# Kernel optimization log

Hardware: AMD Instinct MI355X
Metric: run time of the kernel (lower is better)

## Reference

```python
import jax, jax.numpy as jnp
import numpy as np

B, S, D = 2, 2048, 1024
H, DH = 16, 64  # H*DH == D


def setup_inputs() -> dict:
    key = jax.random.key(0)
    ks = jax.random.split(key, 7)
    scale = 1.0 / np.sqrt(D)
    return {
        "x": jax.random.normal(ks[0], (B, S, D), dtype=jnp.float32),
        "mask": jax.random.normal(ks[1], (B, 1, 1, S), dtype=jnp.float32),
        "Wq": jax.random.normal(ks[2], (D, D), dtype=jnp.float32) * scale,
        "Wk": jax.random.normal(ks[3], (D, D), dtype=jnp.float32) * scale,
        "Wv": jax.random.normal(ks[4], (D, D), dtype=jnp.float32) * scale,
        "Wo": jax.random.normal(ks[5], (D, D), dtype=jnp.float32) * scale,
        "bo": jax.random.normal(ks[6], (D,), dtype=jnp.float32) * 0.01,
    }


def reference(x, mask, Wq, Wk, Wv, Wo, bo):
    # QKV projections (bias-free), split heads: [B,S,D] -> [B,H,S,DH]
    def split_heads(t):
        return t.reshape(B, S, H, DH).transpose(0, 2, 1, 3)

    q = split_heads(x @ Wq)
    k = split_heads(x @ Wk)
    v = split_heads(x @ Wv)

    # NOTE: module scales by sqrt(input_dim), not sqrt(head_size)
    scores = jnp.einsum("bhqd,bhkd->bhqk", q, k) / jnp.sqrt(jnp.float32(D))
    scores = scores + mask  # additive mask, broadcast [B,1,1,S]
    attn = jax.nn.softmax(scores, axis=-1)
    ctx = jnp.einsum("bhqk,bhkd->bhqd", attn, v)  # [B,H,S,DH]
    ctx = ctx.transpose(0, 2, 1, 3).reshape(B, S, H * DH)
    return ctx @ Wo + bo
```

## Files before the change

kernel.cpp:

```cpp
#include <hip/hip_runtime.h>
#include <hip/hip_bf16.h>

#define BB 2
#define SS 2048
#define DD 1024
#define HH 16
#define DHD 64
#define QKLD 2048

typedef __attribute__((ext_vector_type(8))) __bf16 bf16x8;
typedef __attribute__((ext_vector_type(4))) __bf16 bf16x4;
typedef __attribute__((ext_vector_type(4))) float f32x4;

__device__ __forceinline__ f32x4 mfma16(bf16x8 a, bf16x8 b, f32x4 c) {
  return __builtin_amdgcn_mfma_f32_16x16x32_bf16(a, b, c, 0, 0, 0);
}
__device__ __forceinline__ void gload_lds16(const void* g, void* l) {
  __builtin_amdgcn_global_load_lds((__attribute__((address_space(1))) const void*)g,
                                   (__attribute__((address_space(3))) void*)l, 16, 0, 0);
}

__global__ __launch_bounds__(256) void cast_x_em_kernel(
    const float* __restrict__ in, __bf16* __restrict__ out,
    const float* __restrict__ mask, __bf16* __restrict__ embf, int n4) {
  int i = blockIdx.x * 256 + threadIdx.x;
  if (i < n4) {
    float4 f = ((const float4*)in)[i];
    bf16x4 o;
    o[0] = (__bf16)f.x; o[1] = (__bf16)f.y; o[2] = (__bf16)f.z; o[3] = (__bf16)f.w;
    *(bf16x4*)(out + (size_t)i * 4) = o;
  } else {
    int j = i - n4;
    if (j < BB * SS) embf[j] = (__bf16)__expf(mask[j]);
  }
}

__global__ __launch_bounds__(256) void wtrans4_kernel(
    const float* __restrict__ Wq, const float* __restrict__ Wk,
    const float* __restrict__ Wv, const float* __restrict__ Wo,
    __bf16* __restrict__ WTbase) {
  int z = blockIdx.z;
  const float* W = (z == 0) ? Wq : (z == 1) ? Wk : (z == 2) ? Wv : Wo;
  __bf16* WT = WTbase + ((size_t)z << 20);
  __shared__ __bf16 t[64][65];
  int c0 = blockIdx.x * 64, r0 = blockIdx.y * 64;
  int tid = threadIdx.x;
  {
    int rr = tid >> 4, cg = tid & 15;
#pragma unroll
    for (int it = 0; it < 4; ++it) {
      int r = rr + it * 16;
      float4 f = *(const float4*)(W + (size_t)(r0 + r) * DD + c0 + cg * 4);
      t[r][cg * 4 + 0] = (__bf16)f.x;
      t[r][cg * 4 + 1] = (__bf16)f.y;
      t[r][cg * 4 + 2] = (__bf16)f.z;
      t[r][cg * 4 + 3] = (__bf16)f.w;
    }
  }
  __syncthreads();
  {
    int sg = tid & 7;
#pragma unroll
    for (int it = 0; it < 2; ++it) {
      int wc = (tid >> 3) + it * 32;
      __bf16 tmp[8];
#pragma unroll
      for (int e = 0; e < 8; ++e) tmp[e] = t[sg * 8 + e][wc];
      bf16x8 o;
#pragma unroll
      for (int e = 0; e < 8; ++e) o[e] = tmp[e];
      *(bf16x8*)(WT + (size_t)(c0 + wc) * DD + r0 + sg * 8) = o;
    }
  }
}

template <int MODE>
__global__ __launch_bounds__(256, 2) void gemm128_kernel(
    const __bf16* __restrict__ A, const __bf16* __restrict__ BT,
    float* __restrict__ Cf, __bf16* __restrict__ Cb,
    const float* __restrict__ bias, const __bf16* __restrict__ embf,
    int M, int N, int K) {
  __shared__ __bf16 As[2][128 * 32];
  __shared__ __bf16 Bs[2][128 * 32];
  int tid = threadIdx.x;
  int lane = tid & 63, wave = tid >> 6;
  int lr = lane & 15, lg = lane >> 4;
  int wr = wave >> 1, wc = wave & 1;
  int m0 = blockIdx.x * 128, n0 = blockIdx.y * 128;

  int o0 = wave * 1024 + lane * 16;
  int r0i = o0 >> 6, s0i = ((o0 >> 4) & 3) ^ (r0i & 3);
  int o1 = o0 + 4096;
  int r1i = o1 >> 6, s1i = ((o1 >> 4) & 3) ^ (r1i & 3);

  const __bf16* Ag0 = A + (size_t)(m0 + r0i) * K + s0i * 8;
  const __bf16* Ag1 = A + (size_t)(m0 + r1i) * K + s1i * 8;
  const __bf16* Bg0 = BT + (size_t)(n0 + r0i) * K + s0i * 8;
  const __bf16* Bg1 = BT + (size_t)(n0 + r1i) * K + s1i * 8;
  int lb0 = wave * 1024, lb1 = wave * 1024 + 4096;

  f32x4 acc[4][4];
#pragma unroll
  for (int m = 0; m < 4; ++m)
#pragma unroll
    for (int n = 0; n < 4; ++n) acc[m][n] = (f32x4){0.f, 0.f, 0.f, 0.f};

  gload_lds16(Ag0, (char*)As[0] + lb0);
  gload_lds16(Ag1, (char*)As[0] + lb1);
  gload_lds16(Bg0, (char*)Bs[0] + lb0);
  gload_lds16(Bg1, (char*)Bs[0] + lb1);
  __syncthreads();

  int NK = K >> 5;
  for (int it = 0; it < NK; ++it) {
    int cur = it & 1;
    if (it + 1 < NK) {
      int ko = (it + 1) * 32;
      gload_lds16(Ag0 + ko, (char*)As[cur ^ 1] + lb0);
      gload_lds16(Ag1 + ko, (char*)As[cur ^ 1] + lb1);
      gload_lds16(Bg0 + ko, (char*)Bs[cur ^ 1] + lb0);
      gload_lds16(Bg1 + ko, (char*)Bs[cur ^ 1] + lb1);
    }
    const char* Ab = (const char*)As[cur];
    const char* Bb = (const char*)Bs[cur];
    bf16x8 af[4], bfr[4];
#pragma unroll
    for (int m = 0; m < 4; ++m) {
      int row = wr * 64 + m * 16 + lr;
      af[m] = *(const bf16x8*)(Ab + row * 64 + ((lg ^ (row & 3)) << 4));
    }
#pragma unroll
    for (int n = 0; n < 4; ++n) {
      int row = wc * 64 + n * 16 + lr;
      bfr[n] = *(const bf16x8*)(Bb + row * 64 + ((lg ^ (row & 3)) << 4));
    }
#pragma unroll
    for (int m = 0; m < 4; ++m)
#pragma unroll
      for (int n = 0; n < 4; ++n) acc[m][n] = mfma16(af[m], bfr[n], acc[m][n]);
    __syncthreads();
  }

#pragma unroll
  for (int m = 0; m < 4; ++m) {
#pragma unroll
    for (int n = 0; n < 4; ++n) {
      int cc = n0 + wc * 64 + n * 16 + lr;
      float ef = 0.f;
      if constexpr (MODE == 2) ef = (float)embf[cc];
#pragma unroll
      for (int r = 0; r < 4; ++r) {
        int rr = m0 + wr * 64 + m * 16 + 4 * lg + r;
        if constexpr (MODE == 1) {
          Cf[(size_t)rr * N + cc] = acc[m][n][r] + bias[cc];
        } else if constexpr (MODE == 0) {
          Cb[(size_t)rr * N + cc] = (__bf16)acc[m][n][r];
        } else {
          int bb2 = cc >> 11, sl = cc & (SS - 1);
          int hh = rr >> 6, dd2 = rr & 63;
          Cb[(((size_t)bb2 * HH + hh) * DHD + dd2) * SS + sl] =
              (__bf16)(acc[m][n][r] * ef);
        }
      }
    }
  }
}

__global__ __launch_bounds__(256, 2) void attn_kernel(
    const __bf16* __restrict__ QK, const __bf16* __restrict__ VT,
    const __bf16* __restrict__ embf, __bf16* __restrict__ ctxb) {
  __shared__ __bf16 Ks[2][64 * 64];
  __shared__ __bf16 Vs[2][64 * 64];
  __shared__ __attribute__((aligned(16))) __bf16 pS[4][32][72];

  int h = blockIdx.y, b = blockIdx.z;
  int tid = threadIdx.x;
  int wave = tid >> 6, lane = tid & 63;
  int lr = lane & 15, lg = lane >> 4;

  int q0 = blockIdx.x * 128 + wave * 32;
  const __bf16* qp = QK + ((size_t)(b * SS) + q0 + lr) * QKLD + h * DHD;
  bf16x8 qa[2][2];
#pragma unroll
  for (int m = 0; m < 2; ++m)
#pragma unroll
    for (int kc = 0; kc < 2; ++kc)
      qa[m][kc] = *(const bf16x8*)(qp + (size_t)m * 16 * QKLD + kc * 32 + 8 * lg);

  int o0 = tid * 16;
  int row0 = o0 >> 7;
  int ss0 = ((o0 >> 4) & 7) ^ (row0 & 7);
  int lw0 = wave * 1024, lw1 = wave * 1024 + 4096;

  const __bf16* kg = QK + (size_t)(b * SS) * QKLD + DD + h * DHD;
  const __bf16* vg = VT + ((size_t)(b * HH + h) * DHD) * SS;
  const __bf16* Kg0 = kg + (size_t)row0 * QKLD + ss0 * 8;
  const __bf16* Kg1 = kg + (size_t)(row0 + 32) * QKLD + ss0 * 8;
  const __bf16* Vg0 = vg + (size_t)row0 * SS + ss0 * 8;
  const __bf16* Vg1 = vg + (size_t)(row0 + 32) * SS + ss0 * 8;
  const __bf16* ep = embf + b * SS + 8 * lg;

  gload_lds16(Kg0, (char*)Ks[0] + lw0);
  gload_lds16(Kg1, (char*)Ks[0] + lw1);
  gload_lds16(Vg0, (char*)Vs[0] + lw0);
  gload_lds16(Vg1, (char*)Vs[0] + lw1);

  f32x4 ctx[2][4], lacc[2];
#pragma unroll
  for (int m = 0; m < 2; ++m) {
    lacc[m] = (f32x4){0.f, 0.f, 0.f, 0.f};
#pragma unroll
    for (int c = 0; c < 4; ++c) ctx[m][c] = (f32x4){0.f, 0.f, 0.f, 0.f};
  }
  const float SCALE = 0.03125f;
  __syncthreads();

  const int NT = SS / 64;
  for (int it = 0; it < NT; ++it) {
    int cur = it & 1;
    int kb = it * 64;
    if (it + 1 < NT) {
      size_t ko = (size_t)(it + 1) * 64 * QKLD;
      int vo = (it + 1) * 64;
      gload_lds16(Kg0 + ko, (char*)Ks[cur ^ 1] + lw0);
      gload_lds16(Kg1 + ko, (char*)Ks[cur ^ 1] + lw1);
      gload_lds16(Vg0 + vo, (char*)Vs[cur ^ 1] + lw0);
      gload_lds16(Vg1 + vo, (char*)Vs[cur ^ 1] + lw1);
    }
    const char* Kb = (const char*)Ks[cur];
    const char* Vb = (const char*)Vs[cur];
    f32x4 s[2][4];
#pragma unroll
    for (int m = 0; m < 2; ++m)
#pragma unroll
      for (int f = 0; f < 4; ++f) s[m][f] = (f32x4){0.f, 0.f, 0.f, 0.f};
#pragma unroll
    for (int f = 0; f < 4; ++f) {
      int row = f * 16 + lr;
#pragma unroll
      for (int kc = 0; kc < 2; ++kc) {
        bf16x8 kf = *(const bf16x8*)(Kb + row * 128 + (((kc * 4 + lg) ^ (row & 7)) << 4));
#pragma unroll
        for (int m = 0; m < 2; ++m) s[m][f] = mfma16(qa[m][kc], kf, s[m][f]);
      }
    }
#pragma unroll
    for (int m = 0; m < 2; ++m)
#pragma unroll
      for (int f = 0; f < 4; ++f)
#pragma unroll
        for (int r = 0; r < 4; ++r)
          pS[wave][m * 16 + 4 * lg + r][f * 16 + lr] =
              (__bf16)__expf(s[m][f][r] * SCALE);
    bf16x8 emf[2];
    emf[0] = *(const bf16x8*)(ep + kb);
    emf[1] = *(const bf16x8*)(ep + kb + 32);
    bf16x8 pa[2][2];
#pragma unroll
    for (int m = 0; m < 2; ++m)
#pragma unroll
      for (int kc = 0; kc < 2; ++kc)
        pa[m][kc] = *(const bf16x8*)(&pS[wave][m * 16 + lr][kc * 32 + 8 * lg]);
#pragma unroll
    for (int m = 0; m < 2; ++m) {
      lacc[m] = mfma16(pa[m][0], emf[0], lacc[m]);
      lacc[m] = mfma16(pa[m][1], emf[1], lacc[m]);
    }
#pragma unroll
    for (int c = 0; c < 4; ++c) {
      int row = c * 16 + lr;
#pragma unroll
      for (int kc = 0; kc < 2; ++kc) {
        bf16x8 vf = *(const bf16x8*)(Vb + row * 128 + (((kc * 4 + lg) ^ (row & 7)) << 4));
#pragma unroll
        for (int m = 0; m < 2; ++m) ctx[m][c] = mfma16(pa[m][kc], vf, ctx[m][c]);
      }
    }
    __syncthreads();
  }
#pragma unroll
  for (int m = 0; m < 2; ++m) {
    __bf16* op = ctxb + ((size_t)(b * SS) + q0 + m * 16 + 4 * lg) * DD + h * DHD + lr;
#pragma unroll
    for (int r = 0; r < 4; ++r) {
      float inv = 1.0f / lacc[m][r];
#pragma unroll
      for (int c = 0; c < 4; ++c)
        op[(size_t)r * DD + c * 16] = (__bf16)(ctx[m][c][r] * inv);
    }
  }
}

extern "C" void kernel_launch(void* const* d_in, const int* in_sizes, int n_in,
                              void* d_out, int out_size, void* d_ws, size_t ws_size,
                              hipStream_t stream) {
  const float* x    = (const float*)d_in[0];
  const float* mask = (const float*)d_in[1];
  const float* Wq   = (const float*)d_in[2];
  const float* Wk   = (const float*)d_in[3];
  const float* Wv   = (const float*)d_in[4];
  const float* Wo   = (const float*)d_in[5];
  const float* bo   = (const float*)d_in[6];
  float* out = (float*)d_out;

  char* ws = (char*)d_ws;
  const size_t MB = 1024 * 1024;
  __bf16* xb   = (__bf16*)(ws + 0);
  __bf16* WqT  = (__bf16*)(ws + 8 * MB);
  __bf16* WvT  = (__bf16*)(ws + 12 * MB);
  __bf16* WoT  = (__bf16*)(ws + 14 * MB);
  __bf16* qkb  = (__bf16*)(ws + 16 * MB);
  __bf16* vtb  = (__bf16*)(ws + 32 * MB);
  __bf16* embf = (__bf16*)(ws + 40 * MB);
  __bf16* ctxb = xb;

  const int M = BB * SS;
  const int n4 = M * DD / 4;
  cast_x_em_kernel<<<n4 / 256 + 16, 256, 0, stream>>>(x, xb, mask, embf, n4);
  wtrans4_kernel<<<dim3(16, 16, 4), 256, 0, stream>>>(Wq, Wk, Wv, Wo, WqT);
  gemm128_kernel<0><<<dim3(32, 16), 256, 0, stream>>>(
      xb, WqT, nullptr, qkb, nullptr, nullptr, M, 2048, DD);
  gemm128_kernel<2><<<dim3(8, 32), 256, 0, stream>>>(
      WvT, xb, nullptr, vtb, nullptr, embf, DD, M, DD);
  attn_kernel<<<dim3(16, 16, 2), 256, 0, stream>>>(qkb, vtb, embf, ctxb);
  gemm128_kernel<1><<<dim3(32, 8), 256, 0, stream>>>(
      ctxb, WoT, out, nullptr, bo, nullptr, M, DD, DD);
}
```

Baseline: 229.8 us.

## Merge prep and projection launches; split attention across 8 waves of 16 rows

Fuses the cast/mask-exp and weight-transpose kernels into one prep launch, and the QK and V projection GEMMs into one launch that dispatches on block index, cutting the launch count from six to four. Attention blocks now use 512 threads (8 waves), each wave handling 16 query rows instead of 32, so the K/V tile loads are spread over more threads. This raises occupancy and parallelism, but each K/V LDS tile is reused by fewer rows per wave, so LDS reads per MFMA roughly double.

```diff
diff --git a/kernel.cpp b/kernel.cpp
--- a/kernel.cpp
+++ b/kernel.cpp
@@ -20,31 +20,32 @@
                                    (__attribute__((address_space(3))) void*)l, 16, 0, 0);
 }
 
-__global__ __launch_bounds__(256) void cast_x_em_kernel(
-    const float* __restrict__ in, __bf16* __restrict__ out,
-    const float* __restrict__ mask, __bf16* __restrict__ embf, int n4) {
-  int i = blockIdx.x * 256 + threadIdx.x;
-  if (i < n4) {
-    float4 f = ((const float4*)in)[i];
-    bf16x4 o;
-    o[0] = (__bf16)f.x; o[1] = (__bf16)f.y; o[2] = (__bf16)f.z; o[3] = (__bf16)f.w;
-    *(bf16x4*)(out + (size_t)i * 4) = o;
-  } else {
-    int j = i - n4;
-    if (j < BB * SS) embf[j] = (__bf16)__expf(mask[j]);
-  }
-}
-
-__global__ __launch_bounds__(256) void wtrans4_kernel(
+__global__ __launch_bounds__(256) void prep_kernel(
+    const float* __restrict__ x, __bf16* __restrict__ xb,
+    const float* __restrict__ mask, __bf16* __restrict__ embf,
     const float* __restrict__ Wq, const float* __restrict__ Wk,
     const float* __restrict__ Wv, const float* __restrict__ Wo,
     __bf16* __restrict__ WTbase) {
-  int z = blockIdx.z;
+  __shared__ __bf16 t[64][65];
+  int id = blockIdx.x, tid = threadIdx.x;
+  if (id < 4096) {
+    int i = id * 256 + tid;
+    float4 f = ((const float4*)x)[i];
+    bf16x4 o;
+    o[0] = (__bf16)f.x; o[1] = (__bf16)f.y; o[2] = (__bf16)f.z; o[3] = (__bf16)f.w;
+    *(bf16x4*)(xb + (size_t)i * 4) = o;
+    return;
+  }
+  if (id < 4112) {
+    int j = (id - 4096) * 256 + tid;
+    embf[j] = (__bf16)__expf(mask[j]);
+    return;
+  }
+  int idx = id - 4112;
+  int z = idx >> 8, rem = idx & 255;
   const float* W = (z == 0) ? Wq : (z == 1) ? Wk : (z == 2) ? Wv : Wo;
   __bf16* WT = WTbase + ((size_t)z << 20);
-  __shared__ __bf16 t[64][65];
-  int c0 = blockIdx.x * 64, r0 = blockIdx.y * 64;
-  int tid = threadIdx.x;
+  int c0 = (rem & 15) * 64, r0 = (rem >> 4) * 64;
   {
     int rr = tid >> 4, cg = tid & 15;
 #pragma unroll
@@ -75,18 +76,17 @@
 }
 
 template <int MODE>
-__global__ __launch_bounds__(256, 2) void gemm128_kernel(
+__device__ __forceinline__ void gemm_body(
+    char* AsB, char* BsB, int bx, int by,
     const __bf16* __restrict__ A, const __bf16* __restrict__ BT,
     float* __restrict__ Cf, __bf16* __restrict__ Cb,
     const float* __restrict__ bias, const __bf16* __restrict__ embf,
     int M, int N, int K) {
-  __shared__ __bf16 As[2][128 * 32];
-  __shared__ __bf16 Bs[2][128 * 32];
   int tid = threadIdx.x;
   int lane = tid & 63, wave = tid >> 6;
   int lr = lane & 15, lg = lane >> 4;
   int wr = wave >> 1, wc = wave & 1;
-  int m0 = blockIdx.x * 128, n0 = blockIdx.y * 128;
+  int m0 = bx * 128, n0 = by * 128;
 
   int o0 = wave * 1024 + lane * 16;
   int r0i = o0 >> 6, s0i = ((o0 >> 4) & 3) ^ (r0i & 3);
@@ -105,10 +105,10 @@
 #pragma unroll
     for (int n = 0; n < 4; ++n) acc[m][n] = (f32x4){0.f, 0.f, 0.f, 0.f};
 
-  gload_lds16(Ag0, (char*)As[0] + lb0);
-  gload_lds16(Ag1, (char*)As[0] + lb1);
-  gload_lds16(Bg0, (char*)Bs[0] + lb0);
-  gload_lds16(Bg1, (char*)Bs[0] + lb1);
+  gload_lds16(Ag0, AsB + lb0);
+  gload_lds16(Ag1, AsB + lb1);
+  gload_lds16(Bg0, BsB + lb0);
+  gload_lds16(Bg1, BsB + lb1);
   __syncthreads();
 
   int NK = K >> 5;
@@ -116,13 +116,15 @@
     int cur = it & 1;
     if (it + 1 < NK) {
       int ko = (it + 1) * 32;
-      gload_lds16(Ag0 + ko, (char*)As[cur ^ 1] + lb0);
-      gload_lds16(Ag1 + ko, (char*)As[cur ^ 1] + lb1);
-      gload_lds16(Bg0 + ko, (char*)Bs[cur ^ 1] + lb0);
-      gload_lds16(Bg1 + ko, (char*)Bs[cur ^ 1] + lb1);
-    }
-    const char* Ab = (const char*)As[cur];
-    const char* Bb = (const char*)Bs[cur];
+      char* An = AsB + (cur ^ 1) * 8192;
+      char* Bn = BsB + (cur ^ 1) * 8192;
+      gload_lds16(Ag0 + ko, An + lb0);
+      gload_lds16(Ag1 + ko, An + lb1);
+      gload_lds16(Bg0 + ko, Bn + lb0);
+      gload_lds16(Bg1 + ko, Bn + lb1);
+    }
+    const char* Ab = AsB + cur * 8192;
+    const char* Bb = BsB + cur * 8192;
     bf16x8 af[4], bfr[4];
 #pragma unroll
     for (int m = 0; m < 4; ++m) {
@@ -166,52 +168,69 @@
   }
 }
 
-__global__ __launch_bounds__(256, 2) void attn_kernel(
+__global__ __launch_bounds__(256, 2) void proj_kernel(
+    const __bf16* __restrict__ xb, const __bf16* __restrict__ WqT,
+    const __bf16* __restrict__ WvT, __bf16* __restrict__ qkb,
+    __bf16* __restrict__ vtb, const __bf16* __restrict__ embf) {
+  __shared__ __bf16 As[2][128 * 32];
+  __shared__ __bf16 Bs[2][128 * 32];
+  int id = blockIdx.x;
+  if (id < 512) {
+    gemm_body<0>((char*)As, (char*)Bs, id & 31, id >> 5,
+                 xb, WqT, nullptr, qkb, nullptr, nullptr, 4096, 2048, 1024);
+  } else {
+    int i2 = id - 512;
+    gemm_body<2>((char*)As, (char*)Bs, i2 & 7, i2 >> 3,
+                 WvT, xb, nullptr, vtb, nullptr, embf, 1024, 4096, 1024);
+  }
+}
+
+__global__ __launch_bounds__(256, 2) void ogemm_kernel(
+    const __bf16* __restrict__ ctxb, const __bf16* __restrict__ WoT,
+    float* __restrict__ out, const float* __restrict__ bo) {
+  __shared__ __bf16 As[2][128 * 32];
+  __shared__ __bf16 Bs[2][128 * 32];
+  gemm_body<1>((char*)As, (char*)Bs, blockIdx.x, blockIdx.y,
+               ctxb, WoT, out, nullptr, bo, nullptr, 4096, 1024, 1024);
+}
+
+__global__ __launch_bounds__(512, 4) void attn_kernel(
     const __bf16* __restrict__ QK, const __bf16* __restrict__ VT,
     const __bf16* __restrict__ embf, __bf16* __restrict__ ctxb) {
   __shared__ __bf16 Ks[2][64 * 64];
   __shared__ __bf16 Vs[2][64 * 64];
-  __shared__ __attribute__((aligned(16))) __bf16 pS[4][32][72];
+  __shared__ __attribute__((aligned(16))) __bf16 pS[8][16][72];
 
   int h = blockIdx.y, b = blockIdx.z;
   int tid = threadIdx.x;
   int wave = tid >> 6, lane = tid & 63;
   int lr = lane & 15, lg = lane >> 4;
 
-  int q0 = blockIdx.x * 128 + wave * 32;
+  int q0 = blockIdx.x * 128 + wave * 16;
   const __bf16* qp = QK + ((size_t)(b * SS) + q0 + lr) * QKLD + h * DHD;
-  bf16x8 qa[2][2];
-#pragma unroll
-  for (int m = 0; m < 2; ++m)
-#pragma unroll
-    for (int kc = 0; kc < 2; ++kc)
-      qa[m][kc] = *(const bf16x8*)(qp + (size_t)m * 16 * QKLD + kc * 32 + 8 * lg);
+  bf16x8 qa[2];
+#pragma unroll
+  for (int kc = 0; kc < 2; ++kc)
+    qa[kc] = *(const bf16x8*)(qp + kc * 32 + 8 * lg);
 
   int o0 = tid * 16;
   int row0 = o0 >> 7;
   int ss0 = ((o0 >> 4) & 7) ^ (row0 & 7);
-  int lw0 = wave * 1024, lw1 = wave * 1024 + 4096;
+  int lw = wave * 1024;
 
   const __bf16* kg = QK + (size_t)(b * SS) * QKLD + DD + h * DHD;
   const __bf16* vg = VT + ((size_t)(b * HH + h) * DHD) * SS;
   const __bf16* Kg0 = kg + (size_t)row0 * QKLD + ss0 * 8;
-  const __bf16* Kg1 = kg + (size_t)(row0 + 32) * QKLD + ss0 * 8;
   const __bf16* Vg0 = vg + (size_t)row0 * SS + ss0 * 8;
-  const __bf16* Vg1 = vg + (size_t)(row0 + 32) * SS + ss0 * 8;
   const __bf16* ep = embf + b * SS + 8 * lg;
 
-  gload_lds16(Kg0, (char*)Ks[0] + lw0);
-  gload_lds16(Kg1, (char*)Ks[0] + lw1);
-  gload_lds16(Vg0, (char*)Vs[0] + lw0);
-  gload_lds16(Vg1, (char*)Vs[0] + lw1);
-
-  f32x4 ctx[2][4], lacc[2];
-#pragma unroll
-  for (int m = 0; m < 2; ++m) {
-    lacc[m] = (f32x4){0.f, 0.f, 0.f, 0.f};
-#pragma unroll
-    for (int c = 0; c < 4; ++c) ctx[m][c] = (f32x4){0.f, 0.f, 0.f, 0.f};
-  }
+  gload_lds16(Kg0, (char*)Ks[0] + lw);
+  gload_lds16(Vg0, (char*)Vs[0] + lw);
+
+  f32x4 ctx[4], lacc;
+  lacc = (f32x4){0.f, 0.f, 0.f, 0.f};
+#pragma unroll
+  for (int c = 0; c < 4; ++c) ctx[c] = (f32x4){0.f, 0.f, 0.f, 0.f};
   const float SCALE = 0.03125f;
   __syncthreads();
 
@@ -222,72 +241,55 @@
     if (it + 1 < NT) {
       size_t ko = (size_t)(it + 1) * 64 * QKLD;
       int vo = (it + 1) * 64;
-      gload_lds16(Kg0 + ko, (char*)Ks[cur ^ 1] + lw0);
-      gload_lds16(Kg1 + ko, (char*)Ks[cur ^ 1] + lw1);
-      gload_lds16(Vg0 + vo, (char*)Vs[cur ^ 1] + lw0);
-      gload_lds16(Vg1 + vo, (char*)Vs[cur ^ 1] + lw1);
+      gload_lds16(Kg0 + ko, (char*)Ks[cur ^ 1] + lw);
+      gload_lds16(Vg0 + vo, (char*)Vs[cur ^ 1] + lw);
     }
     const char* Kb = (const char*)Ks[cur];
     const char* Vb = (const char*)Vs[cur];
-    f32x4 s[2][4];
-#pragma unroll
-    for (int m = 0; m < 2; ++m)
-#pragma unroll
-      for (int f = 0; f < 4; ++f) s[m][f] = (f32x4){0.f, 0.f, 0.f, 0.f};
+    f32x4 s[4];
+#pragma unroll
+    for (int f = 0; f < 4; ++f) s[f] = (f32x4){0.f, 0.f, 0.f, 0.f};
 #pragma unroll
     for (int f = 0; f < 4; ++f) {
       int row = f * 16 + lr;
 #pragma unroll
       for (int kc = 0; kc < 2; ++kc) {
         bf16x8 kf = *(const bf16x8*)(Kb + row * 128 + (((kc * 4 + lg) ^ (row & 7)) << 4));
-#pragma unroll
-        for (int m = 0; m < 2; ++m) s[m][f] = mfma16(qa[m][kc], kf, s[m][f]);
+        s[f] = mfma16(qa[kc], kf, s[f]);
       }
     }
 #pragma unroll
-    for (int m = 0; m < 2; ++m)
-#pragma unroll
-      for (int f = 0; f < 4; ++f)
-#pragma unroll
-        for (int r = 0; r < 4; ++r)
-          pS[wave][m * 16 + 4 * lg + r][f * 16 + lr] =
-              (__bf16)__expf(s[m][f][r] * SCALE);
+    for (int f = 0; f < 4; ++f)
+#pragma unroll
+      for (int r = 0; r < 4; ++r)
+        pS[wave][4 * lg + r][f * 16 + lr] = (__bf16)__expf(s[f][r] * SCALE);
     bf16x8 emf[2];
     emf[0] = *(const bf16x8*)(ep + kb);
     emf[1] = *(const bf16x8*)(ep + kb + 32);
-    bf16x8 pa[2][2];
-#pragma unroll
-    for (int m = 0; m < 2; ++m)
-#pragma unroll
-      for (int kc = 0; kc < 2; ++kc)
-        pa[m][kc] = *(const bf16x8*)(&pS[wave][m * 16 + lr][kc * 32 + 8 * lg]);
-#pragma unroll
-    for (int m = 0; m < 2; ++m) {
-      lacc[m] = mfma16(pa[m][0], emf[0], lacc[m]);
-      lacc[m] = mfma16(pa[m][1], emf[1], lacc[m]);
-    }
+    bf16x8 pa[2];
+#pragma unroll
+    for (int kc = 0; kc < 2; ++kc)
+      pa[kc] = *(const bf16x8*)(&pS[wave][lr][kc * 32 + 8 * lg]);
+    lacc = mfma16(pa[0], emf[0], lacc);
+    lacc = mfma16(pa[1], emf[1], lacc);
 #pragma unroll
     for (int c = 0; c < 4; ++c) {
       int row = c * 16 + lr;
 #pragma unroll
       for (int kc = 0; kc < 2; ++kc) {
         bf16x8 vf = *(const bf16x8*)(Vb + row * 128 + (((kc * 4 + lg) ^ (row & 7)) << 4));
-#pragma unroll
-        for (int m = 0; m < 2; ++m) ctx[m][c] = mfma16(pa[m][kc], vf, ctx[m][c]);
+        ctx[c] = mfma16(pa[kc], vf, ctx[c]);
       }
     }
     __syncthreads();
   }
-#pragma unroll
-  for (int m = 0; m < 2; ++m) {
-    __bf16* op = ctxb + ((size_t)(b * SS) + q0 + m * 16 + 4 * lg) * DD + h * DHD + lr;
-#pragma unroll
-    for (int r = 0; r < 4; ++r) {
-      float inv = 1.0f / lacc[m][r];
-#pragma unroll
-      for (int c = 0; c < 4; ++c)
-        op[(size_t)r * DD + c * 16] = (__bf16)(ctx[m][c][r] * inv);
-    }
+  __bf16* op = ctxb + ((size_t)(b * SS) + q0 + 4 * lg) * DD + h * DHD + lr;
+#pragma unroll
+  for (int r = 0; r < 4; ++r) {
+    float inv = 1.0f / lacc[r];
+#pragma unroll
+    for (int c = 0; c < 4; ++c)
+      op[(size_t)r * DD + c * 16] = (__bf16)(ctx[c][r] * inv);
   }
 }
 
@@ -314,15 +316,8 @@
   __bf16* embf = (__bf16*)(ws + 40 * MB);
   __bf16* ctxb = xb;
 
-  const int M = BB * SS;
-  const int n4 = M * DD / 4;
-  cast_x_em_kernel<<<n4 / 256 + 16, 256, 0, stream>>>(x, xb, mask, embf, n4);
-  wtrans4_kernel<<<dim3(16, 16, 4), 256, 0, stream>>>(Wq, Wk, Wv, Wo, WqT);
-  gemm128_kernel<0><<<dim3(32, 16), 256, 0, stream>>>(
-      xb, WqT, nullptr, qkb, nullptr, nullptr, M, 2048, DD);
-  gemm128_kernel<2><<<dim3(8, 32), 256, 0, stream>>>(
-      WvT, xb, nullptr, vtb, nullptr, embf, DD, M, DD);
-  attn_kernel<<<dim3(16, 16, 2), 256, 0, stream>>>(qkb, vtb, embf, ctxb);
-  gemm128_kernel<1><<<dim3(32, 8), 256, 0, stream>>>(
-      ctxb, WoT, out, nullptr, bo, nullptr, M, DD, DD);
-}
+  prep_kernel<<<5136, 256, 0, stream>>>(x, xb, mask, embf, Wq, Wk, Wv, Wo, WqT);
+  proj_kernel<<<768, 256, 0, stream>>>(xb, WqT, WvT, qkb, vtb, embf);
+  attn_kernel<<<dim3(16, HH, BB), 512, 0, stream>>>(qkb, vtb, embf, ctxb);
+  ogemm_kernel<<<dim3(32, 8), 256, 0, stream>>>(ctxb, WoT, out, bo);
+}
```

New measurement: 212.9 us. 1.08x faster.
